# Kernel optimization log

Measured on AMD Instinct MI355X. Metric: run time of the kernel, lower is better.

Reference implementation:

```python
import jax, jax.numpy as jnp
import numpy as np

B, S, D = 4, 2048, 1024
H, HK = 16, 4          # num_heads, num_heads_kv
HD = D // H            # head_dim = 64
G = H // HK            # kv groups = 4


def setup_inputs() -> dict:
    key = jax.random.key(0)
    ks = jax.random.split(key, 7)
    s = 0.02
    return {
        "query": jax.random.normal(ks[0], (B, S, D), jnp.float32),
        "key":   jax.random.normal(ks[1], (B, S, D), jnp.float32),
        "value": jax.random.normal(ks[2], (B, S, D), jnp.float32),
        # weights stored (in, out); equivalent to torch Linear y = x @ W.T
        "Wq": jax.random.normal(ks[3], (D, H * HD), jnp.float32) * s,
        "Wk": jax.random.normal(ks[4], (D, HK * HD), jnp.float32) * s,
        "Wv": jax.random.normal(ks[5], (D, HK * HD), jnp.float32) * s,
        "Wo": jax.random.normal(ks[6], (H * HD, D), jnp.float32) * s,
    }


def reference(query, key, value, Wq, Wk, Wv, Wo):
    b, qlen, _ = query.shape
    kvlen = key.shape[1]
    # projections
    q = (query @ Wq).reshape(b, qlen, H, HD)        # [b,q,H,hd]
    k = (key @ Wk).reshape(b, kvlen, HK, HD)        # [b,s,HK,hd]
    v = (value @ Wv).reshape(b, kvlen, HK, HD)      # [b,s,HK,hd]
    # GQA: q head h attends kv head h//G (repeat_interleave semantics)
    qg = q.reshape(b, qlen, HK, G, HD)              # head = kv*G + group
    scale = 1.0 / jnp.sqrt(jnp.asarray(HD, q.dtype))
    # scores [b,HK,G,q,s] -- broadcast kv heads, no materialized repeat
    scores = jnp.einsum('bqkgd,bskd->bkgqs', qg, k) * scale
    attn = jax.nn.softmax(scores, axis=-1)
    out = jnp.einsum('bkgqs,bskd->bqkgd', attn, v)  # [b,q,HK,G,hd]
    out = out.reshape(b, qlen, H * HD)
    return out @ Wo
```

## Files before the change

### kernel.cpp

```cpp
#include <hip/hip_runtime.h>


typedef unsigned short u16;
typedef unsigned int   u32;
typedef __bf16 bf16x4 __attribute__((ext_vector_type(4)));
typedef __bf16 bf16x8 __attribute__((ext_vector_type(8)));
typedef float  f32x4  __attribute__((ext_vector_type(4)));

#define MFMA(a,b,c) __builtin_amdgcn_mfma_f32_16x16x32_bf16((a),(b),(c),0,0,0)

#define GLDS(g, l) __builtin_amdgcn_global_load_lds(                          \
    (const __attribute__((address_space(1))) void*)(g),                       \
    (__attribute__((address_space(3))) void*)(l), 16, 0, 0)

#if __has_builtin(__builtin_amdgcn_exp2f)
#define EXP2(x) __builtin_amdgcn_exp2f(x)
#else
#define EXP2(x) exp2f(x)
#endif

__device__ __forceinline__ u16 f2bf(float f){
    u32 u = __builtin_bit_cast(u32, f);
    u += 0x7fffu + ((u >> 16) & 1u);
    return (u16)(u >> 16);
}
__device__ __forceinline__ u32 pk2(float a, float b){
#if __has_builtin(__builtin_amdgcn_cvt_pk_bf16_f32)
    auto r = __builtin_amdgcn_cvt_pk_bf16_f32(a, b);
    return __builtin_bit_cast(u32, r);
#else
    return (u32)f2bf(a) | ((u32)f2bf(b) << 16);
#endif
}
__device__ __forceinline__ bf16x8 ldfrag(const u16* p){
    return *(const bf16x8*)p;
}
__device__ __forceinline__ bf16x8 ld2x64(const u16* p){
    bf16x4 lo = *(const bf16x4*)p;
    bf16x4 hi = *(const bf16x4*)(p + 4);
    bf16x8 r;
    r[0]=lo[0]; r[1]=lo[1]; r[2]=lo[2]; r[3]=lo[3];
    r[4]=hi[0]; r[5]=hi[1]; r[6]=hi[2]; r[7]=hi[3];
    return r;
}

__global__ __launch_bounds__(256) void prep(const float* __restrict__ q,
                                            const float* __restrict__ k,
                                            const float* __restrict__ v,
                                            const float* __restrict__ Wq,
                                            const float* __restrict__ Wk,
                                            const float* __restrict__ Wv,
                                            const float* __restrict__ Wo,
                                            u16* Qc, u16* Kc, u16* Vc,
                                            u16* WqT, u16* WkT, u16* WvT, u16* WoT){
    const int tid = threadIdx.x, bid = blockIdx.x;
    if (bid < 2560){
        __shared__ float T[32][33];
        const float* W; u16* WT; int N, i;
        if (bid < 1024)      { W = Wq; WT = WqT; N = 1024; i = bid; }
        else if (bid < 1280) { W = Wk; WT = WkT; N =  256; i = bid - 1024; }
        else if (bid < 1536) { W = Wv; WT = WvT; N =  256; i = bid - 1280; }
        else                 { W = Wo; WT = WoT; N = 1024; i = bid - 1536; }
        int kt = (i & 31) * 32, nt = (i >> 5) * 32;
        int r = tid >> 3, c = tid & 7;
        float4 vv = *(const float4*)(W + (size_t)(kt + r) * N + nt + c * 4);
        T[r][c*4+0] = vv.x; T[r][c*4+1] = vv.y; T[r][c*4+2] = vv.z; T[r][c*4+3] = vv.w;
        __syncthreads();
        u32 lo = pk2(T[c*4+0][r], T[c*4+1][r]);
        u32 hi = pk2(T[c*4+2][r], T[c*4+3][r]);
        *(uint2*)(WT + (size_t)(nt + r) * 1024 + kt + c * 4) = make_uint2(lo, hi);
    } else {
        int i = bid - 2560;
        const float* src = (i < 512) ? q : (i < 1024 ? k : v);
        u16*         dst = (i < 512) ? Qc : (i < 1024 ? Kc : Vc);
        size_t off = (size_t)(i & 511) * 16384;
        const float* s = src + off;
        u16* d = dst + off;
        #pragma unroll
        for (int p = 0; p < 16; ++p){
            int idx = (p * 256 + tid) * 4;
            float4 vv = *(const float4*)(s + idx);
            *(uint2*)(d + idx) = make_uint2(pk2(vv.x, vv.y), pk2(vv.z, vv.w));
        }
    }
}

template<int EPI>
__device__ __forceinline__ void gemm_body(const u16* __restrict__ A,
                                          const u16* __restrict__ Bt,
                                          void* __restrict__ Cp,
                                          int N, int K, int m0, int n0,
                                          u16* As, u16* Bs, float oscale){
    const int tid  = threadIdx.x;
    const int wave = tid >> 6, lane = tid & 63;
    const int quad = lane >> 4, l15 = lane & 15;
    const int wm = wave >> 1, wn = wave & 1;
    const int srow = lane >> 3;
    const int scol = ((lane & 7) ^ srow) * 8;
    const int swz  = l15 & 7;

    f32x4 acc[4][4];
    #pragma unroll
    for (int i = 0; i < 4; ++i)
        #pragma unroll
        for (int j = 0; j < 4; ++j) acc[i][j] = (f32x4){0.f, 0.f, 0.f, 0.f};

    const int nkt = K >> 6;
    for (int kt = 0; kt < nkt; ++kt){
        __syncthreads();
        {
            const u16* ga = A + (size_t)(m0 + wave*32 + srow) * K + kt*64 + scol;
            u16* la = As + (wave*32) * 64;
            #pragma unroll
            for (int p = 0; p < 4; ++p)
                GLDS(ga + (size_t)(p*8) * K, la + p*8*64);
            const u16* gb = Bt + (size_t)(n0 + wave*32 + srow) * K + kt*64 + scol;
            u16* lb = Bs + (wave*32) * 64;
            #pragma unroll
            for (int p = 0; p < 4; ++p)
                GLDS(gb + (size_t)(p*8) * K, lb + p*8*64);
        }
        __syncthreads();
        #pragma unroll
        for (int ks = 0; ks < 2; ++ks){
            bf16x8 af[4], bfr[4];
            #pragma unroll
            for (int mt = 0; mt < 4; ++mt)
                af[mt] = ldfrag(&As[(wm*64 + mt*16 + l15) * 64 +
                                    (((ks*4 + quad) ^ swz) * 8)]);
            #pragma unroll
            for (int nt = 0; nt < 4; ++nt)
                bfr[nt] = ldfrag(&Bs[(wn*64 + nt*16 + l15) * 64 +
                                     (((ks*4 + quad) ^ swz) * 8)]);
            #pragma unroll
            for (int mt = 0; mt < 4; ++mt)
                #pragma unroll
                for (int nt = 0; nt < 4; ++nt){
                    if constexpr (EPI == 1)
                        acc[mt][nt] = MFMA(af[mt], bfr[nt], acc[mt][nt]);
                    else
                        acc[mt][nt] = MFMA(bfr[nt], af[mt], acc[mt][nt]);
                }
        }
    }
    #pragma unroll
    for (int mt = 0; mt < 4; ++mt){
        #pragma unroll
        for (int nt = 0; nt < 4; ++nt){
            if constexpr (EPI == 1){
                int rowb = m0 + wm*64 + mt*16 + quad*4;
                int col  = n0 + wn*64 + nt*16 + l15;
                u16* C = (u16*)Cp;
                int bb = rowb >> 11, s = rowb & 2047;
                u32 lo = pk2(acc[mt][nt][0], acc[mt][nt][1]);
                u32 hi = pk2(acc[mt][nt][2], acc[mt][nt][3]);
                *(uint2*)(C + (size_t)(bb * 256 + col) * 2048 + s) = make_uint2(lo, hi);
            } else {
                int row  = m0 + wm*64 + mt*16 + l15;
                int colb = n0 + wn*64 + nt*16 + quad*4;
                if constexpr (EPI == 0){
                    u16* C = (u16*)Cp;
                    u32 lo = pk2(acc[mt][nt][0]*oscale, acc[mt][nt][1]*oscale);
                    u32 hi = pk2(acc[mt][nt][2]*oscale, acc[mt][nt][3]*oscale);
                    *(uint2*)(C + (size_t)row * N + colb) = make_uint2(lo, hi);
                } else {
                    float* C = (float*)Cp;
                    *(f32x4*)(C + (size_t)row * N + colb) = acc[mt][nt];
                }
            }
        }
    }
}

__global__ __launch_bounds__(256) void gemm_qkv(const u16* Qc, const u16* WqT, u16* Qp,
                                                const u16* Kc, const u16* WkT, u16* Kp,
                                                const u16* Vc, const u16* WvT, u16* Vt,
                                                float qscale){
    __shared__ u16 As[128 * 64];
    __shared__ u16 Bs[128 * 64];
    int bid = blockIdx.x;
    if (bid < 512)
        gemm_body<0>(Qc, WqT, Qp, 1024, 1024, (bid >> 3) * 128, (bid & 7) * 128,
                     As, Bs, qscale);
    else if (bid < 640){
        int i = bid - 512;
        gemm_body<0>(Kc, WkT, Kp, 256, 1024, (i >> 1) * 128, (i & 1) * 128,
                     As, Bs, 1.0f);
    } else {
        int i = bid - 640;
        gemm_body<1>(Vc, WvT, Vt, 256, 1024, (i >> 1) * 128, (i & 1) * 128,
                     As, Bs, 1.0f);
    }
}

__global__ __launch_bounds__(256) void gemm_o(const u16* AO, const u16* WoT,
                                              float* Out){
    __shared__ u16 As[128 * 64];
    __shared__ u16 Bs[128 * 64];
    int bid = blockIdx.x;
    gemm_body<2>(AO, WoT, Out, 1024, 1024, (bid >> 3) * 128, (bid & 7) * 128,
                 As, Bs, 1.0f);
}

__global__ __launch_bounds__(256) void attn_k(const u16* __restrict__ Qp,
                                              const u16* __restrict__ Kp,
                                              const u16* __restrict__ Vt,
                                              u16* __restrict__ AO){
    constexpr int S = 2048, Dm = 1024, NKV = 256, PST = 68;
    __shared__ u16 Kb[2][64 * 64];
    __shared__ u16 Vb[2][64 * 64];
    __shared__ u16 Ps[256 * PST];
    const int tid = threadIdx.x, wave = tid >> 6, lane = tid & 63;
    const int quad = lane >> 4, l15 = lane & 15;
    const int h = blockIdx.y, b = blockIdx.z;
    const int hk = h >> 2, q0 = blockIdx.x * 256;
    u16* pw = Ps + wave * (64 * PST);

    const int srow = lane >> 3;
    const int scol = ((lane & 7) ^ srow) * 8;
    const int swz  = l15 & 7;

    auto issue = [&](int t){
        int j0 = t * 64, bufi = t & 1;
        #pragma unroll
        for (int p = 0; p < 2; ++p){
            int r = wave * 16 + p * 8 + srow;
            GLDS(Kp + (size_t)(b * S + j0 + r) * NKV + hk * 64 + scol,
                 &Kb[bufi][(wave * 16 + p * 8) * 64]);
            GLDS(Vt + (size_t)(b * NKV + hk * 64 + r) * S + j0 + scol,
                 &Vb[bufi][(wave * 16 + p * 8) * 64]);
        }
    };

    issue(0);
    {
        int c8 = tid & 7, r0 = tid >> 3;
        #pragma unroll
        for (int p = 0; p < 8; ++p){
            int r = r0 + p * 32;
            uint4 v = *(const uint4*)(Qp + (size_t)(b * S + q0 + r) * Dm + h * 64 + c8 * 8);
            *(uint2*)&Ps[r * PST + c8 * 8]     = make_uint2(v.x, v.y);
            *(uint2*)&Ps[r * PST + c8 * 8 + 4] = make_uint2(v.z, v.w);
        }
    }
    __syncthreads();
    bf16x8 qf[4][2];
    #pragma unroll
    for (int mt = 0; mt < 4; ++mt)
        #pragma unroll
        for (int ks = 0; ks < 2; ++ks)
            qf[mt][ks] = ld2x64(&Ps[(wave*64 + mt*16 + l15) * PST + ks*32 + quad*8]);

    const u32 one2 = 0x3F803F80u;
    const bf16x8 ones = __builtin_bit_cast(bf16x8, make_uint4(one2, one2, one2, one2));

    f32x4 O[4][4];
    #pragma unroll
    for (int dt = 0; dt < 4; ++dt)
        #pragma unroll
        for (int mt = 0; mt < 4; ++mt) O[dt][mt] = (f32x4){0.f, 0.f, 0.f, 0.f};
    f32x4 sums[4];
    #pragma unroll
    for (int mt = 0; mt < 4; ++mt) sums[mt] = (f32x4){0.f, 0.f, 0.f, 0.f};

    for (int t = 0; t < 32; ++t){
        __syncthreads();
        if (t < 31) issue(t + 1);
        const u16* Kt = Kb[t & 1];
        const u16* Vs = Vb[t & 1];
        bf16x8 ak[2][4];
        #pragma unroll
        for (int ks = 0; ks < 2; ++ks)
            #pragma unroll
            for (int nt = 0; nt < 4; ++nt)
                ak[ks][nt] = ldfrag(&Kt[(nt*16 + l15) * 64 + (((ks*4 + quad) ^ swz) * 8)]);
        #pragma unroll
        for (int mt = 0; mt < 4; ++mt){
            f32x4 sf[4];
            #pragma unroll
            for (int nt = 0; nt < 4; ++nt) sf[nt] = (f32x4){0.f, 0.f, 0.f, 0.f};
            #pragma unroll
            for (int ks = 0; ks < 2; ++ks)
                #pragma unroll
                for (int nt = 0; nt < 4; ++nt)
                    sf[nt] = MFMA(ak[ks][nt], qf[mt][ks], sf[nt]);
            #pragma unroll
            for (int nt = 0; nt < 4; ++nt){
                float e0 = EXP2(sf[nt][0]);
                float e1 = EXP2(sf[nt][1]);
                float e2 = EXP2(sf[nt][2]);
                float e3 = EXP2(sf[nt][3]);
                *(uint2*)&pw[(mt*16 + l15) * PST + nt*16 + quad*4] =
                    make_uint2(pk2(e0, e1), pk2(e2, e3));
            }
        }
        __threadfence_block();
        #pragma unroll
        for (int ks = 0; ks < 2; ++ks){
            bf16x8 av[4], bp[4];
            #pragma unroll
            for (int dt = 0; dt < 4; ++dt)
                av[dt] = ldfrag(&Vs[(dt*16 + l15) * 64 + (((ks*4 + quad) ^ swz) * 8)]);
            #pragma unroll
            for (int mt = 0; mt < 4; ++mt)
                bp[mt] = ld2x64(&pw[(mt*16 + l15) * PST + ks*32 + quad*8]);
            #pragma unroll
            for (int mt = 0; mt < 4; ++mt)
                sums[mt] = MFMA(ones, bp[mt], sums[mt]);
            #pragma unroll
            for (int dt = 0; dt < 4; ++dt)
                #pragma unroll
                for (int mt = 0; mt < 4; ++mt)
                    O[dt][mt] = MFMA(av[dt], bp[mt], O[dt][mt]);
        }
    }
    #pragma unroll
    for (int mt = 0; mt < 4; ++mt){
        float inv = 1.0f / sums[mt][0];
        size_t row = (size_t)(b * S + q0 + wave*64 + mt*16 + l15);
        #pragma unroll
        for (int dt = 0; dt < 4; ++dt){
            u32 lo = pk2(O[dt][mt][0] * inv, O[dt][mt][1] * inv);
            u32 hi = pk2(O[dt][mt][2] * inv, O[dt][mt][3] * inv);
            *(uint2*)(AO + row * Dm + h * 64 + dt*16 + quad*4) = make_uint2(lo, hi);
        }
    }
}

extern "C" void kernel_launch(void* const* d_in, const int* in_sizes, int n_in,
                              void* d_out, int out_size, void* d_ws, size_t ws_size,
                              hipStream_t stream){
    const float* q  = (const float*)d_in[0];
    const float* k  = (const float*)d_in[1];
    const float* v  = (const float*)d_in[2];
    const float* Wq = (const float*)d_in[3];
    const float* Wk = (const float*)d_in[4];
    const float* Wv = (const float*)d_in[5];
    const float* Wo = (const float*)d_in[6];
    char* ws = (char*)d_ws;
    const size_t MB = 1u << 20;
    u16* WqT = (u16*)(ws);
    u16* WkT = (u16*)(ws + 2*MB);
    u16* WvT = (u16*)(ws + 2*MB + 512*1024);
    u16* WoT = (u16*)(ws + 3*MB);
    u16* Qc  = (u16*)(ws + 5*MB);
    u16* Kc  = (u16*)(ws + 21*MB);
    u16* Vc  = (u16*)(ws + 37*MB);
    u16* Qp  = (u16*)(ws + 53*MB);
    u16* Kp  = (u16*)(ws + 69*MB);
    u16* Vt  = (u16*)(ws + 73*MB);
    u16* AO  = (u16*)(ws + 5*MB);

    const float cexp = 0.125f * 1.44269504f;

    prep<<<dim3(4096), 256, 0, stream>>>(q, k, v, Wq, Wk, Wv, Wo,
                                         Qc, Kc, Vc, WqT, WkT, WvT, WoT);
    gemm_qkv<<<dim3(768), 256, 0, stream>>>(Qc, WqT, Qp, Kc, WkT, Kp,
                                            Vc, WvT, Vt, cexp);
    attn_k<<<dim3(8, 16, 4), 256, 0, stream>>>(Qp, Kp, Vt, AO);
    gemm_o<<<dim3(512), 256, 0, stream>>>(AO, WoT, (float*)d_out);
}
```

Measured before the change: 367.6 us.

## Split attention work across eight waves with 32 query rows each

The attention kernel now launches 512 threads per block instead of 256. Each wave handles 32 query rows instead of 64, and the K/V tile loads are spread across the eight waves. Accumulator and Q fragment registers are halved to raise occupancy and hide latency. In exchange, each K/V LDS fragment load is amortised over fewer MFMAs, and block-wide barriers now synchronise more waves.

```diff
diff --git a/kernel.cpp b/kernel.cpp
--- a/kernel.cpp
+++ b/kernel.cpp
@@ -202,10 +202,10 @@
                  As, Bs, 1.0f);
 }
 
-__global__ __launch_bounds__(256) void attn_k(const u16* __restrict__ Qp,
-                                              const u16* __restrict__ Kp,
-                                              const u16* __restrict__ Vt,
-                                              u16* __restrict__ AO){
+__global__ __launch_bounds__(512, 4) void attn_k(const u16* __restrict__ Qp,
+                                                 const u16* __restrict__ Kp,
+                                                 const u16* __restrict__ Vt,
+                                                 u16* __restrict__ AO){
     constexpr int S = 2048, Dm = 1024, NKV = 256, PST = 68;
     __shared__ u16 Kb[2][64 * 64];
     __shared__ u16 Vb[2][64 * 64];
@@ -214,7 +214,7 @@
     const int quad = lane >> 4, l15 = lane & 15;
     const int h = blockIdx.y, b = blockIdx.z;
     const int hk = h >> 2, q0 = blockIdx.x * 256;
-    u16* pw = Ps + wave * (64 * PST);
+    u16* pw = Ps + wave * (32 * PST);
 
     const int srow = lane >> 3;
     const int scol = ((lane & 7) ^ srow) * 8;
@@ -222,102 +222,101 @@
 
     auto issue = [&](int t){
         int j0 = t * 64, bufi = t & 1;
-        #pragma unroll
-        for (int p = 0; p < 2; ++p){
-            int r = wave * 16 + p * 8 + srow;
-            GLDS(Kp + (size_t)(b * S + j0 + r) * NKV + hk * 64 + scol,
-                 &Kb[bufi][(wave * 16 + p * 8) * 64]);
-            GLDS(Vt + (size_t)(b * NKV + hk * 64 + r) * S + j0 + scol,
-                 &Vb[bufi][(wave * 16 + p * 8) * 64]);
-        }
+        int r = wave * 8 + srow;
+        GLDS(Kp + (size_t)(b * S + j0 + r) * NKV + hk * 64 + scol,
+             &Kb[bufi][wave * 8 * 64]);
+        GLDS(Vt + (size_t)(b * NKV + hk * 64 + r) * S + j0 + scol,
+             &Vb[bufi][wave * 8 * 64]);
     };
 
     issue(0);
     {
         int c8 = tid & 7, r0 = tid >> 3;
         #pragma unroll
-        for (int p = 0; p < 8; ++p){
-            int r = r0 + p * 32;
+        for (int p = 0; p < 4; ++p){
+            int r = r0 + p * 64;
             uint4 v = *(const uint4*)(Qp + (size_t)(b * S + q0 + r) * Dm + h * 64 + c8 * 8);
             *(uint2*)&Ps[r * PST + c8 * 8]     = make_uint2(v.x, v.y);
             *(uint2*)&Ps[r * PST + c8 * 8 + 4] = make_uint2(v.z, v.w);
         }
     }
     __syncthreads();
-    bf16x8 qf[4][2];
-    #pragma unroll
-    for (int mt = 0; mt < 4; ++mt)
+    bf16x8 qf[2][2];
+    #pragma unroll
+    for (int mt = 0; mt < 2; ++mt)
         #pragma unroll
         for (int ks = 0; ks < 2; ++ks)
-            qf[mt][ks] = ld2x64(&Ps[(wave*64 + mt*16 + l15) * PST + ks*32 + quad*8]);
+            qf[mt][ks] = ld2x64(&Ps[(wave*32 + mt*16 + l15) * PST + ks*32 + quad*8]);
 
     const u32 one2 = 0x3F803F80u;
     const bf16x8 ones = __builtin_bit_cast(bf16x8, make_uint4(one2, one2, one2, one2));
 
-    f32x4 O[4][4];
+    f32x4 O[4][2];
     #pragma unroll
     for (int dt = 0; dt < 4; ++dt)
         #pragma unroll
-        for (int mt = 0; mt < 4; ++mt) O[dt][mt] = (f32x4){0.f, 0.f, 0.f, 0.f};
-    f32x4 sums[4];
-    #pragma unroll
-    for (int mt = 0; mt < 4; ++mt) sums[mt] = (f32x4){0.f, 0.f, 0.f, 0.f};
+        for (int mt = 0; mt < 2; ++mt) O[dt][mt] = (f32x4){0.f, 0.f, 0.f, 0.f};
+    f32x4 sums[2];
+    #pragma unroll
+    for (int mt = 0; mt < 2; ++mt) sums[mt] = (f32x4){0.f, 0.f, 0.f, 0.f};
 
     for (int t = 0; t < 32; ++t){
         __syncthreads();
         if (t < 31) issue(t + 1);
         const u16* Kt = Kb[t & 1];
         const u16* Vs = Vb[t & 1];
-        bf16x8 ak[2][4];
-        #pragma unroll
-        for (int ks = 0; ks < 2; ++ks)
+        f32x4 sf[2][4];
+        #pragma unroll
+        for (int mt = 0; mt < 2; ++mt)
+            #pragma unroll
+            for (int nt = 0; nt < 4; ++nt) sf[mt][nt] = (f32x4){0.f, 0.f, 0.f, 0.f};
+        #pragma unroll
+        for (int ks = 0; ks < 2; ++ks){
+            bf16x8 ak[4];
             #pragma unroll
             for (int nt = 0; nt < 4; ++nt)
-                ak[ks][nt] = ldfrag(&Kt[(nt*16 + l15) * 64 + (((ks*4 + quad) ^ swz) * 8)]);
-        #pragma unroll
-        for (int mt = 0; mt < 4; ++mt){
-            f32x4 sf[4];
-            #pragma unroll
-            for (int nt = 0; nt < 4; ++nt) sf[nt] = (f32x4){0.f, 0.f, 0.f, 0.f};
-            #pragma unroll
-            for (int ks = 0; ks < 2; ++ks)
+                ak[nt] = ldfrag(&Kt[(nt*16 + l15) * 64 + (((ks*4 + quad) ^ swz) * 8)]);
+            #pragma unroll
+            for (int mt = 0; mt < 2; ++mt)
                 #pragma unroll
                 for (int nt = 0; nt < 4; ++nt)
-                    sf[nt] = MFMA(ak[ks][nt], qf[mt][ks], sf[nt]);
+                    sf[mt][nt] = MFMA(ak[nt], qf[mt][ks], sf[mt][nt]);
+        }
+        #pragma unroll
+        for (int mt = 0; mt < 2; ++mt)
             #pragma unroll
             for (int nt = 0; nt < 4; ++nt){
-                float e0 = EXP2(sf[nt][0]);
-                float e1 = EXP2(sf[nt][1]);
-                float e2 = EXP2(sf[nt][2]);
-                float e3 = EXP2(sf[nt][3]);
+                float e0 = EXP2(sf[mt][nt][0]);
+                float e1 = EXP2(sf[mt][nt][1]);
+                float e2 = EXP2(sf[mt][nt][2]);
+                float e3 = EXP2(sf[mt][nt][3]);
                 *(uint2*)&pw[(mt*16 + l15) * PST + nt*16 + quad*4] =
                     make_uint2(pk2(e0, e1), pk2(e2, e3));
             }
-        }
         __threadfence_block();
         #pragma unroll
         for (int ks = 0; ks < 2; ++ks){
-            bf16x8 av[4], bp[4];
+            bf16x8 av[4], bp[2];
             #pragma unroll
             for (int dt = 0; dt < 4; ++dt)
                 av[dt] = ldfrag(&Vs[(dt*16 + l15) * 64 + (((ks*4 + quad) ^ swz) * 8)]);
             #pragma unroll
-            for (int mt = 0; mt < 4; ++mt)
+            for (int mt = 0; mt < 2; ++mt)
                 bp[mt] = ld2x64(&pw[(mt*16 + l15) * PST + ks*32 + quad*8]);
             #pragma unroll
-            for (int mt = 0; mt < 4; ++mt)
+            for (int mt = 0; mt < 2; ++mt)
                 sums[mt] = MFMA(ones, bp[mt], sums[mt]);
             #pragma unroll
             for (int dt = 0; dt < 4; ++dt)
                 #pragma unroll
-                for (int mt = 0; mt < 4; ++mt)
+                for (int mt = 0; mt < 2; ++mt)
                     O[dt][mt] = MFMA(av[dt], bp[mt], O[dt][mt]);
         }
     }
     #pragma unroll
-    for (int mt = 0; mt < 4; ++mt){
+    for (int mt = 0; mt < 2; ++mt){
         float inv = 1.0f / sums[mt][0];
-        size_t row = (size_t)(b * S + q0 + wave*64 + mt*16 + l15);
+        size_t row = (size_t)(b * S + q0 + wave*32 + mt*16 + l15);
         #pragma unroll
         for (int dt = 0; dt < 4; ++dt){
             u32 lo = pk2(O[dt][mt][0] * inv, O[dt][mt][1] * inv);
@@ -357,6 +356,6 @@
                                          Qc, Kc, Vc, WqT, WkT, WvT, WoT);
     gemm_qkv<<<dim3(768), 256, 0, stream>>>(Qc, WqT, Qp, Kc, WkT, Kp,
                                             Vc, WvT, Vt, cexp);
-    attn_k<<<dim3(8, 16, 4), 256, 0, stream>>>(Qp, Kp, Vt, AO);
+    attn_k<<<dim3(8, 16, 4), 512, 0, stream>>>(Qp, Kp, Vt, AO);
     gemm_o<<<dim3(512), 256, 0, stream>>>(AO, WoT, (float*)d_out);
 }
```

After: 315.0 us. 14.3% less time.
